# Optimization experiments

Measured on AMD Instinct MI355X. Metric: run time of the kernel, lower is better.

The kernel has to match this reference:

```python
import jax, jax.numpy as jnp
import numpy as np

N_NODES = 50000
N_EDGES = 800000


def setup_inputs() -> dict:
    key = jax.random.key(0)
    ks = jax.random.split(key, 10)
    x = jax.random.normal(ks[0], (N_NODES, 256), dtype=jnp.float32)
    edge_index = jax.random.randint(ks[1], (2, N_EDGES), 0, N_NODES, dtype=jnp.int64)
    edge_attr = jax.random.uniform(ks[2], (N_EDGES,), dtype=jnp.float32)
    def glorot(k, fan_in, fan_out):
        s = jnp.sqrt(6.0 / (fan_in + fan_out))
        return jax.random.uniform(k, (fan_in, fan_out), minval=-s, maxval=s, dtype=jnp.float32)
    W1 = glorot(ks[3], 256, 512); b1 = jnp.zeros((512,), jnp.float32)
    W2 = glorot(ks[4], 512, 256); b2 = jnp.zeros((256,), jnp.float32)
    W3 = glorot(ks[5], 256, 128); b3 = jnp.zeros((128,), jnp.float32)
    return {"x": x, "edge_index": edge_index, "edge_attr": edge_attr,
            "W1": W1, "b1": b1, "W2": W2, "b2": b2, "W3": W3, "b3": b3}


def _gcn_norm(edge_index, edge_attr, num_nodes):
    # PyG GCNConv default: add self-loops (weight 1), symmetric normalization.
    loops = jnp.arange(num_nodes, dtype=edge_index.dtype)
    src = jnp.concatenate([edge_index[0], loops])
    dst = jnp.concatenate([edge_index[1], loops])
    w = jnp.concatenate([edge_attr, jnp.ones((num_nodes,), edge_attr.dtype)])
    deg = jax.ops.segment_sum(w, dst, num_segments=num_nodes)
    dinv = jnp.where(deg > 0, jax.lax.rsqrt(deg), 0.0)
    norm = dinv[src] * w * dinv[dst]  # [E+N]
    return src, dst, norm


def _gcn_conv(h, W, b, src, dst, norm, num_nodes):
    h = h @ W                                   # [N, Dout] linear transform
    msg = h[src] * norm[:, None]                # gather + per-edge scale
    out = jax.ops.segment_sum(msg, dst, num_segments=num_nodes)  # scatter-add
    return out + b


def reference(x, edge_index, edge_attr, W1, b1, W2, b2, W3, b3):
    src, dst, norm = _gcn_norm(edge_index, edge_attr, N_NODES)
    h = jax.nn.relu(_gcn_conv(x, W1, b1, src, dst, norm, N_NODES))
    # dropout is identity in eval mode (reference runs with training=False)
    h = jax.nn.relu(_gcn_conv(h, W2, b2, src, dst, norm, N_NODES))
    h = _gcn_conv(h, W3, b3, src, dst, norm, N_NODES)
    return h.reshape(-1, h.shape[1])
```

## Files before the change

kernel.cpp:

```cpp
#include <hip/hip_runtime.h>
#include <cstdint>
#include <cstddef>

typedef unsigned short u16;
typedef unsigned int u32;

#define NN 50000
#define NE 800000

typedef __attribute__((ext_vector_type(8))) short bf16x8;
typedef __attribute__((ext_vector_type(4))) float f32x4;

__device__ __forceinline__ u16 f2bf(float f) {
  union { float f; u32 i; } v; v.f = f;
  return (u16)((v.i + 0x7FFFu + ((v.i >> 16) & 1u)) >> 16);
}
__device__ __forceinline__ void bf2x2(u32 w, float& a, float& b) {
  union { u32 i; float f; } lo, hi;
  lo.i = w << 16; hi.i = w & 0xFFFF0000u;
  a = lo.f; b = hi.f;
}
__device__ __forceinline__ void unpack8(const uint4& q, float* f) {
  bf2x2(q.x, f[0], f[1]); bf2x2(q.y, f[2], f[3]);
  bf2x2(q.z, f[4], f[5]); bf2x2(q.w, f[6], f[7]);
}

__global__ void k_hist(int* __restrict__ cnt, const int* __restrict__ dst, int E) {
  int e = blockIdx.x * 256 + threadIdx.x;
  if (e < E) atomicAdd(&cnt[dst[e]], 1);
}
__global__ void k_scan_part(const int* __restrict__ cnt, int* __restrict__ bsum, int n) {
  __shared__ int s[256];
  int i = blockIdx.x * 256 + threadIdx.x;
  s[threadIdx.x] = (i < n) ? cnt[i] : 0;
  __syncthreads();
  for (int o = 128; o > 0; o >>= 1) {
    if (threadIdx.x < o) s[threadIdx.x] += s[threadIdx.x + o];
    __syncthreads();
  }
  if (threadIdx.x == 0) bsum[blockIdx.x] = s[0];
}
__global__ void k_scan_fin(const int* __restrict__ cnt, const int* __restrict__ bsum,
                           int* __restrict__ rowptr, int* __restrict__ cursor, int n) {
  __shared__ int s[256];
  __shared__ int pre[256];
  int t = threadIdx.x;
  int i = blockIdx.x * 256 + t;
  pre[t] = (t < blockIdx.x) ? bsum[t] : 0;
  s[t] = (i < n) ? cnt[i] : 0;
  __syncthreads();
  for (int o = 128; o > 0; o >>= 1) {
    if (t < o) pre[t] += pre[t + o];
    __syncthreads();
  }
  if (t == 0) {
    int run = pre[0];
    for (int j = 0; j < 256; j++) { int v = s[j]; s[j] = run; run += v; }
  }
  __syncthreads();
  if (i < n) { rowptr[i] = s[t]; cursor[i] = s[t]; }
}
__global__ void k_fill(const int* __restrict__ src, const int* __restrict__ dst,
                       const float* __restrict__ w,
                       int* __restrict__ cursor, uint2* __restrict__ edges, int E) {
  int e = blockIdx.x * 256 + threadIdx.x;
  if (e < E) {
    int d = dst[e];
    int p = atomicAdd(&cursor[d], 1);
    uint2 ev;
    ev.x = (u32)src[e];
    ev.y = __float_as_uint(w[e]);
    edges[p] = ev;
  }
}

__global__ __launch_bounds__(256) void k_sortrow(
    uint2* __restrict__ edges, const int* __restrict__ rowptr,
    const int* __restrict__ cnt, float* __restrict__ dinv, int n) {
  int wave = threadIdx.x >> 6, lane = threadIdx.x & 63;
  int row = blockIdx.x * 4 + wave;
  if (row >= n) return;
  int p = rowptr[row], c = cnt[row];
  if (c <= 64) {
    u32 kc = 0xFFFFFFFFu, kw = 0xFFFFFFFFu;
    if (lane < c) { uint2 e = edges[p + lane]; kc = e.x; kw = e.y; }
#pragma unroll
    for (int k = 2; k <= 64; k <<= 1) {
#pragma unroll
      for (int j = k >> 1; j > 0; j >>= 1) {
        u32 oc = __shfl_xor(kc, j, 64);
        u32 ow = __shfl_xor(kw, j, 64);
        bool up = ((lane & k) == 0);
        bool lower = ((lane & j) == 0);
        bool gt = (kc > oc) || (kc == oc && kw > ow);
        bool lt = (kc < oc) || (kc == oc && kw < ow);
        bool swap = up ? (lower ? gt : lt) : (lower ? lt : gt);
        if (swap) { kc = oc; kw = ow; }
      }
    }
    float s = (lane < c) ? __uint_as_float(kw) : 0.f;
#pragma unroll
    for (int off = 1; off < 64; off <<= 1) s += __shfl_xor(s, off, 64);
    if (lane < c) { uint2 e; e.x = kc; e.y = kw; edges[p + lane] = e; }
    if (lane == 0) dinv[row] = rsqrtf(1.0f + s);
  } else {
    if (lane == 0) {
      for (int i = 1; i < c; i++) {
        uint2 key = edges[p + i];
        int j2 = i - 1;
        while (j2 >= 0) {
          uint2 a = edges[p + j2];
          bool gt = (a.x > key.x) || (a.x == key.x && a.y > key.y);
          if (!gt) break;
          edges[p + j2 + 1] = a; j2--;
        }
        edges[p + j2 + 1] = key;
      }
      float s = 0.f;
      for (int i = 0; i < c; i++) s += __uint_as_float(edges[p + i].y);
      dinv[row] = rsqrtf(1.0f + s);
    }
  }
}

__global__ __launch_bounds__(256) void k_val(
    uint2* __restrict__ edges, const int* __restrict__ rowptr,
    const int* __restrict__ cnt, const float* __restrict__ dinv, int n) {
  int wave = threadIdx.x >> 6, lane = threadIdx.x & 63;
  int row = blockIdx.x * 4 + wave;
  if (row >= n) return;
  int p = rowptr[row], c = cnt[row];
  float dr = dinv[row];
  for (int l = lane; l < c; l += 64) {
    uint2 e = edges[p + l];
    float w = __uint_as_float(e.y);
    e.y = __float_as_uint(dinv[(int)e.x] * w * dr);
    edges[p + l] = e;
  }
}

#define XGROUPS (NN * 256 / 4)
__global__ void k_cast_all(const float* __restrict__ x, const float* __restrict__ W1,
                           const float* __restrict__ W2, const float* __restrict__ W3,
                           u16* __restrict__ xb, u16* __restrict__ Wt1,
                           u16* __restrict__ Wt2, u16* __restrict__ Wt3) {
  int i = blockIdx.x * 256 + threadIdx.x;
  if (i < XGROUPS) {
    float4 f = ((const float4*)x)[i];
    uint2 u;
    u.x = (u32)f2bf(f.x) | ((u32)f2bf(f.y) << 16);
    u.y = (u32)f2bf(f.z) | ((u32)f2bf(f.w) << 16);
    ((uint2*)xb)[i] = u;
  } else {
    int j = i - XGROUPS;
    if (j < 131072) {
      int k = j >> 9, n = j & 511;
      Wt1[n * 256 + k] = f2bf(W1[j]);
    } else if (j < 262144) {
      int j2 = j - 131072;
      int k = j2 >> 8, n = j2 & 255;
      Wt2[n * 512 + k] = f2bf(W2[j2]);
    } else if (j < 294912) {
      int j2 = j - 262144;
      int k = j2 >> 7, n = j2 & 127;
      Wt3[n * 256 + k] = f2bf(W3[j2]);
    }
  }
}

template <int D, int OUTF32, int RELU, int HASB, int U>
__global__ __launch_bounds__(128) void k_agg(
    const u16* __restrict__ H, const int* __restrict__ rowptr,
    const int* __restrict__ cnt, const uint2* __restrict__ edges,
    const float* __restrict__ dinv,
    const float* __restrict__ bias, void* __restrict__ outv) {
  constexpr int RL = D / 8;
  constexpr int EPW = 64 / RL;
  int wave = threadIdx.x >> 6, lane = threadIdx.x & 63;
  int node = blockIdx.x * 2 + wave;
  if (node >= NN) return;
  const int sub = lane / RL;
  const int rl = lane & (RL - 1);
  const int base = rl * 8;
  float acc[8] = {};
  if (sub == 0) {
    float dv = dinv[node];
    float sw = dv * dv;
    uint4 q = *(const uint4*)(H + (size_t)node * D + base);
    float f[8]; unpack8(q, f);
#pragma unroll
    for (int j = 0; j < 8; j++) acc[j] = sw * f[j];
  }
  const int p = rowptr[node], c = cnt[node];
  for (int e0 = 0; e0 < c; e0 += EPW * U) {
    uint4 q[U];
    float v[U];
#pragma unroll
    for (int u = 0; u < U; u++) {
      int id = e0 + sub + u * EPW;
      bool ok = id < c;
      uint2 ev = edges[p + (ok ? id : 0)];
      v[u] = ok ? __uint_as_float(ev.y) : 0.f;
      int cs = ok ? (int)ev.x : node;
      q[u] = *(const uint4*)(H + (size_t)cs * D + base);
    }
#pragma unroll
    for (int u = 0; u < U; u++) {
      float f[8]; unpack8(q[u], f);
#pragma unroll
      for (int j = 0; j < 8; j++) acc[j] += v[u] * f[j];
    }
  }
#pragma unroll
  for (int j = 0; j < 8; j++) {
#pragma unroll
    for (int off = RL; off < 64; off <<= 1)
      acc[j] += __shfl_xor(acc[j], off, 64);
  }
  if (sub == 0) {
#pragma unroll
    for (int j = 0; j < 8; j++) {
      float v2 = acc[j];
      if (HASB) v2 += bias[base + j];
      if (RELU) v2 = fmaxf(v2, 0.f);
      acc[j] = v2;
    }
    if (OUTF32) {
      float* o = (float*)outv + (size_t)node * D + base;
      float4 f0 = {acc[0], acc[1], acc[2], acc[3]};
      float4 f1 = {acc[4], acc[5], acc[6], acc[7]};
      *(float4*)o = f0;
      *(float4*)(o + 4) = f1;
    } else {
      u16* o = (u16*)outv + (size_t)node * D + base;
      uint4 u;
      u.x = (u32)f2bf(acc[0]) | ((u32)f2bf(acc[1]) << 16);
      u.y = (u32)f2bf(acc[2]) | ((u32)f2bf(acc[3]) << 16);
      u.z = (u32)f2bf(acc[4]) | ((u32)f2bf(acc[5]) << 16);
      u.w = (u32)f2bf(acc[6]) | ((u32)f2bf(acc[7]) << 16);
      *(uint4*)o = u;
    }
  }
}

template <int RELU, int HASB>
__global__ __launch_bounds__(512) void k_gemm(
    const u16* __restrict__ A, const u16* __restrict__ Bt,
    const float* __restrict__ bias, u16* __restrict__ C, int M, int Nd, int K) {
  __shared__ u16 As[256 * 64];
  __shared__ u16 Bs[128 * 64];
  const int tid = threadIdx.x;
  const int wave = tid >> 6, lane = tid & 63;
  const int m0 = blockIdx.x * 256, n0 = blockIdx.y * 128;
  const int wr = wave >> 1, wc = wave & 1;
  f32x4 acc[4][4] = {};

  for (int k0 = 0; k0 < K; k0 += 64) {
#pragma unroll
    for (int i = 0; i < 4; i++) {
      int r = i * 64 + wave * 8 + (lane >> 3);
      int rg = m0 + r; rg = rg < M ? rg : M - 1;
      const u16* ga = A + (size_t)rg * K + k0 + (lane & 7) * 8;
      __builtin_amdgcn_global_load_lds(
          (const __attribute__((address_space(1))) void*)ga,
          (__attribute__((address_space(3))) void*)&As[(i * 64 + wave * 8) * 64], 16, 0, 0);
    }
#pragma unroll
    for (int i = 0; i < 2; i++) {
      int r = i * 64 + wave * 8 + (lane >> 3);
      int ng = n0 + r;
      const u16* gb = Bt + (size_t)ng * K + k0 + (lane & 7) * 8;
      __builtin_amdgcn_global_load_lds(
          (const __attribute__((address_space(1))) void*)gb,
          (__attribute__((address_space(3))) void*)&Bs[(i * 64 + wave * 8) * 64], 16, 0, 0);
    }
    __syncthreads();
#pragma unroll
    for (int kk = 0; kk < 2; kk++) {
      bf16x8 af[4], bfr[4];
#pragma unroll
      for (int mi = 0; mi < 4; mi++)
        af[mi] = *(const bf16x8*)&As[(wr * 64 + mi * 16 + (lane & 15)) * 64 + kk * 32 + (lane >> 4) * 8];
#pragma unroll
      for (int ni = 0; ni < 4; ni++)
        bfr[ni] = *(const bf16x8*)&Bs[(wc * 64 + ni * 16 + (lane & 15)) * 64 + kk * 32 + (lane >> 4) * 8];
#pragma unroll
      for (int mi = 0; mi < 4; mi++)
#pragma unroll
        for (int ni = 0; ni < 4; ni++)
          acc[mi][ni] = __builtin_amdgcn_mfma_f32_16x16x32_bf16(af[mi], bfr[ni], acc[mi][ni], 0, 0, 0);
    }
    __syncthreads();
  }
  const int nb = n0 + wc * 64 + (lane & 15);
  float bv[4];
#pragma unroll
  for (int ni = 0; ni < 4; ni++) bv[ni] = HASB ? bias[nb + ni * 16] : 0.f;
#pragma unroll
  for (int mi = 0; mi < 4; mi++) {
#pragma unroll
    for (int r = 0; r < 4; r++) {
      int row = m0 + wr * 64 + mi * 16 + (lane >> 4) * 4 + r;
      if (row < M) {
#pragma unroll
        for (int ni = 0; ni < 4; ni++) {
          float v = acc[mi][ni][r] + bv[ni];
          if (RELU) v = fmaxf(v, 0.f);
          C[(size_t)row * Nd + nb + ni * 16] = f2bf(v);
        }
      }
    }
  }
}

extern "C" void kernel_launch(void* const* d_in, const int* in_sizes, int n_in,
                              void* d_out, int out_size, void* d_ws, size_t ws_size,
                              hipStream_t stream) {
  const float* x  = (const float*)d_in[0];
  const int*   ei = (const int*)d_in[1];
  const float* ea = (const float*)d_in[2];
  const float* W1 = (const float*)d_in[3];
  const float* b1 = (const float*)d_in[4];
  const float* W2 = (const float*)d_in[5];
  const float* b2 = (const float*)d_in[6];
  const float* W3 = (const float*)d_in[7];
  const float* b3 = (const float*)d_in[8];
  const int* e_src = ei;
  const int* e_dst = ei + NE;

  size_t off = 0;
  auto carve = [&](size_t bytes) -> void* {
    void* r = (char*)d_ws + off;
    off += (bytes + 255) & ~(size_t)255;
    return r;
  };
  float* dinv   = (float*)carve(NN * 4);
  int*   counts = (int*)carve(NN * 4);
  int*   rowptr = (int*)carve(NN * 4);
  int*   cursor = (int*)carve(NN * 4);
  int*   bsum   = (int*)carve(256 * 4);
  uint2* edges  = (uint2*)carve((size_t)NE * 8);
  u16*   Wt1    = (u16*)carve(512 * 256 * 2);
  u16*   Wt2    = (u16*)carve(256 * 512 * 2);
  u16*   Wt3    = (u16*)carve(128 * 256 * 2);
  u16*   R0     = (u16*)carve((size_t)NN * 256 * 2);
  u16*   R1     = (u16*)carve((size_t)NN * 256 * 2);
  u16*   R2     = (u16*)carve((size_t)NN * 512 * 2);

  const int NB_N = (NN + 255) / 256;
  const int NB_E = (NE + 255) / 256;
  const int ROW_B = (NN + 3) / 4;
  const int AGG_B = (NN + 1) / 2;

  hipMemsetAsync(counts, 0, (size_t)NN * 4, stream);
  k_hist<<<NB_E, 256, 0, stream>>>(counts, e_dst, NE);
  k_scan_part<<<NB_N, 256, 0, stream>>>(counts, bsum, NN);
  k_scan_fin<<<NB_N, 256, 0, stream>>>(counts, bsum, rowptr, cursor, NN);
  k_fill<<<NB_E, 256, 0, stream>>>(e_src, e_dst, ea, cursor, edges, NE);
  k_sortrow<<<ROW_B, 256, 0, stream>>>(edges, rowptr, counts, dinv, NN);
  k_val<<<ROW_B, 256, 0, stream>>>(edges, rowptr, counts, dinv, NN);

  k_cast_all<<<(XGROUPS + 294912 + 255) / 256, 256, 0, stream>>>(
      x, W1, W2, W3, R0, Wt1, Wt2, Wt3);

  dim3 g1((NN + 255) / 256, 512 / 128);
  dim3 g2((NN + 255) / 256, 256 / 128);
  dim3 g3((NN + 255) / 256, 128 / 128);

  k_agg<256, 0, 0, 0, 4><<<AGG_B, 128, 0, stream>>>(R0, rowptr, counts, edges, dinv, nullptr, R1);
  k_gemm<1, 1><<<g1, 512, 0, stream>>>(R1, Wt1, b1, R2, NN, 512, 256);
  k_gemm<0, 0><<<g2, 512, 0, stream>>>(R2, Wt2, nullptr, R0, NN, 256, 512);
  k_agg<256, 0, 1, 1, 4><<<AGG_B, 128, 0, stream>>>(R0, rowptr, counts, edges, dinv, b2, R1);
  k_gemm<0, 0><<<g3, 512, 0, stream>>>(R1, Wt3, nullptr, R0, NN, 128, 256);
  k_agg<128, 1, 0, 1, 4><<<AGG_B, 128, 0, stream>>>(R0, rowptr, counts, edges, dinv, b3, d_out);
}
```

Baseline: 391.0 us.

## Fuse degree computation into histogram, normalize in fill, remap GEMM blocks across XCDs

Computes weighted degree during the histogram pass with deterministic fixed-point 64-bit atomics, merges the bf16 cast kernel into that launch, and computes dinv in the scan kernel. Edge normalization now happens in k_fill, which removes the separate k_val pass and the degree reduction inside the sort. The GEMMs use a 1D grid with an XCD-aware block remapping so neighbouring tiles share an L2. This cuts kernel launches and passes over the edge array, at the cost of 64-bit atomics and double-precision conversions per edge.

Result: no change. 396.9 us (+1.5%).

```diff
diff --git a/kernel.cpp b/kernel.cpp
--- a/kernel.cpp
+++ b/kernel.cpp
@@ -4,6 +4,7 @@
 
 typedef unsigned short u16;
 typedef unsigned int u32;
+typedef unsigned long long u64;
 
 #define NN 50000
 #define NE 800000
@@ -25,10 +26,51 @@
   bf2x2(q.z, f[4], f[5]); bf2x2(q.w, f[6], f[7]);
 }
 
-__global__ void k_hist(int* __restrict__ cnt, const int* __restrict__ dst, int E) {
-  int e = blockIdx.x * 256 + threadIdx.x;
-  if (e < E) atomicAdd(&cnt[dst[e]], 1);
-}
+#define HIST_B 3125
+#define XGROUPS (NN * 256 / 4)
+#define DEGSCALE 1099511627776.0
+
+__global__ void k_histdeg_cast(const int* __restrict__ dst, const float* __restrict__ w,
+                               int* __restrict__ cnt, u64* __restrict__ degfix,
+                               const float* __restrict__ x, const float* __restrict__ W1,
+                               const float* __restrict__ W2, const float* __restrict__ W3,
+                               u16* __restrict__ xb, u16* __restrict__ Wt1,
+                               u16* __restrict__ Wt2, u16* __restrict__ Wt3) {
+  int b = blockIdx.x;
+  if (b < HIST_B) {
+    int e = b * 256 + threadIdx.x;
+    if (e < NE) {
+      int d = dst[e];
+      atomicAdd(&cnt[d], 1);
+      u64 fx = (u64)((double)w[e] * DEGSCALE + 0.5);
+      atomicAdd(&degfix[d], fx);
+    }
+  } else {
+    int i = (b - HIST_B) * 256 + threadIdx.x;
+    if (i < XGROUPS) {
+      float4 f = ((const float4*)x)[i];
+      uint2 u;
+      u.x = (u32)f2bf(f.x) | ((u32)f2bf(f.y) << 16);
+      u.y = (u32)f2bf(f.z) | ((u32)f2bf(f.w) << 16);
+      ((uint2*)xb)[i] = u;
+    } else {
+      int j = i - XGROUPS;
+      if (j < 131072) {
+        int k = j >> 9, n = j & 511;
+        Wt1[n * 256 + k] = f2bf(W1[j]);
+      } else if (j < 262144) {
+        int j2 = j - 131072;
+        int k = j2 >> 8, n = j2 & 255;
+        Wt2[n * 512 + k] = f2bf(W2[j2]);
+      } else if (j < 294912) {
+        int j2 = j - 262144;
+        int k = j2 >> 7, n = j2 & 127;
+        Wt3[n * 256 + k] = f2bf(W3[j2]);
+      }
+    }
+  }
+}
+
 __global__ void k_scan_part(const int* __restrict__ cnt, int* __restrict__ bsum, int n) {
   __shared__ int s[256];
   int i = blockIdx.x * 256 + threadIdx.x;
@@ -41,7 +83,9 @@
   if (threadIdx.x == 0) bsum[blockIdx.x] = s[0];
 }
 __global__ void k_scan_fin(const int* __restrict__ cnt, const int* __restrict__ bsum,
-                           int* __restrict__ rowptr, int* __restrict__ cursor, int n) {
+                           const u64* __restrict__ degfix,
+                           int* __restrict__ rowptr, int* __restrict__ cursor,
+                           float* __restrict__ dinv, int n) {
   __shared__ int s[256];
   __shared__ int pre[256];
   int t = threadIdx.x;
@@ -58,25 +102,30 @@
     for (int j = 0; j < 256; j++) { int v = s[j]; s[j] = run; run += v; }
   }
   __syncthreads();
-  if (i < n) { rowptr[i] = s[t]; cursor[i] = s[t]; }
+  if (i < n) {
+    rowptr[i] = s[t];
+    cursor[i] = s[t];
+    double dg = 1.0 + (double)degfix[i] * (1.0 / DEGSCALE);
+    dinv[i] = rsqrtf((float)dg);
+  }
 }
 __global__ void k_fill(const int* __restrict__ src, const int* __restrict__ dst,
-                       const float* __restrict__ w,
+                       const float* __restrict__ w, const float* __restrict__ dinv,
                        int* __restrict__ cursor, uint2* __restrict__ edges, int E) {
   int e = blockIdx.x * 256 + threadIdx.x;
   if (e < E) {
-    int d = dst[e];
+    int d = dst[e], s0 = src[e];
     int p = atomicAdd(&cursor[d], 1);
     uint2 ev;
-    ev.x = (u32)src[e];
-    ev.y = __float_as_uint(w[e]);
+    ev.x = (u32)s0;
+    ev.y = __float_as_uint(dinv[s0] * w[e] * dinv[d]);
     edges[p] = ev;
   }
 }
 
 __global__ __launch_bounds__(256) void k_sortrow(
     uint2* __restrict__ edges, const int* __restrict__ rowptr,
-    const int* __restrict__ cnt, float* __restrict__ dinv, int n) {
+    const int* __restrict__ cnt, int n) {
   int wave = threadIdx.x >> 6, lane = threadIdx.x & 63;
   int row = blockIdx.x * 4 + wave;
   if (row >= n) return;
@@ -98,11 +147,7 @@
         if (swap) { kc = oc; kw = ow; }
       }
     }
-    float s = (lane < c) ? __uint_as_float(kw) : 0.f;
-#pragma unroll
-    for (int off = 1; off < 64; off <<= 1) s += __shfl_xor(s, off, 64);
     if (lane < c) { uint2 e; e.x = kc; e.y = kw; edges[p + lane] = e; }
-    if (lane == 0) dinv[row] = rsqrtf(1.0f + s);
   } else {
     if (lane == 0) {
       for (int i = 1; i < c; i++) {
@@ -116,54 +161,6 @@
         }
         edges[p + j2 + 1] = key;
       }
-      float s = 0.f;
-      for (int i = 0; i < c; i++) s += __uint_as_float(edges[p + i].y);
-      dinv[row] = rsqrtf(1.0f + s);
-    }
-  }
-}
-
-__global__ __launch_bounds__(256) void k_val(
-    uint2* __restrict__ edges, const int* __restrict__ rowptr,
-    const int* __restrict__ cnt, const float* __restrict__ dinv, int n) {
-  int wave = threadIdx.x >> 6, lane = threadIdx.x & 63;
-  int row = blockIdx.x * 4 + wave;
-  if (row >= n) return;
-  int p = rowptr[row], c = cnt[row];
-  float dr = dinv[row];
-  for (int l = lane; l < c; l += 64) {
-    uint2 e = edges[p + l];
-    float w = __uint_as_float(e.y);
-    e.y = __float_as_uint(dinv[(int)e.x] * w * dr);
-    edges[p + l] = e;
-  }
-}
-
-#define XGROUPS (NN * 256 / 4)
-__global__ void k_cast_all(const float* __restrict__ x, const float* __restrict__ W1,
-                           const float* __restrict__ W2, const float* __restrict__ W3,
-                           u16* __restrict__ xb, u16* __restrict__ Wt1,
-                           u16* __restrict__ Wt2, u16* __restrict__ Wt3) {
-  int i = blockIdx.x * 256 + threadIdx.x;
-  if (i < XGROUPS) {
-    float4 f = ((const float4*)x)[i];
-    uint2 u;
-    u.x = (u32)f2bf(f.x) | ((u32)f2bf(f.y) << 16);
-    u.y = (u32)f2bf(f.z) | ((u32)f2bf(f.w) << 16);
-    ((uint2*)xb)[i] = u;
-  } else {
-    int j = i - XGROUPS;
-    if (j < 131072) {
-      int k = j >> 9, n = j & 511;
-      Wt1[n * 256 + k] = f2bf(W1[j]);
-    } else if (j < 262144) {
-      int j2 = j - 131072;
-      int k = j2 >> 8, n = j2 & 255;
-      Wt2[n * 512 + k] = f2bf(W2[j2]);
-    } else if (j < 294912) {
-      int j2 = j - 262144;
-      int k = j2 >> 7, n = j2 & 127;
-      Wt3[n * 256 + k] = f2bf(W3[j2]);
     }
   }
 }
@@ -243,7 +240,7 @@
   }
 }
 
-template <int RELU, int HASB>
+template <int RELU, int HASB, int NYB>
 __global__ __launch_bounds__(512) void k_gemm(
     const u16* __restrict__ A, const u16* __restrict__ Bt,
     const float* __restrict__ bias, u16* __restrict__ C, int M, int Nd, int K) {
@@ -251,15 +248,20 @@
   __shared__ u16 Bs[128 * 64];
   const int tid = threadIdx.x;
   const int wave = tid >> 6, lane = tid & 63;
-  const int m0 = blockIdx.x * 256, n0 = blockIdx.y * 128;
+  const int nwg = gridDim.x;
+  const int orig = blockIdx.x;
+  const int xcd = orig & 7;
+  const int q = nwg >> 3, r = nwg & 7;
+  const int wgid = (xcd < r ? xcd * (q + 1) : r * (q + 1) + (xcd - r) * q) + (orig >> 3);
+  const int m0 = (wgid / NYB) * 256, n0 = (wgid % NYB) * 128;
   const int wr = wave >> 1, wc = wave & 1;
   f32x4 acc[4][4] = {};
 
   for (int k0 = 0; k0 < K; k0 += 64) {
 #pragma unroll
     for (int i = 0; i < 4; i++) {
-      int r = i * 64 + wave * 8 + (lane >> 3);
-      int rg = m0 + r; rg = rg < M ? rg : M - 1;
+      int rr = i * 64 + wave * 8 + (lane >> 3);
+      int rg = m0 + rr; rg = rg < M ? rg : M - 1;
       const u16* ga = A + (size_t)rg * K + k0 + (lane & 7) * 8;
       __builtin_amdgcn_global_load_lds(
           (const __attribute__((address_space(1))) void*)ga,
@@ -267,8 +269,8 @@
     }
 #pragma unroll
     for (int i = 0; i < 2; i++) {
-      int r = i * 64 + wave * 8 + (lane >> 3);
-      int ng = n0 + r;
+      int rr = i * 64 + wave * 8 + (lane >> 3);
+      int ng = n0 + rr;
       const u16* gb = Bt + (size_t)ng * K + k0 + (lane & 7) * 8;
       __builtin_amdgcn_global_load_lds(
           (const __attribute__((address_space(1))) void*)gb,
@@ -299,12 +301,12 @@
 #pragma unroll
   for (int mi = 0; mi < 4; mi++) {
 #pragma unroll
-    for (int r = 0; r < 4; r++) {
-      int row = m0 + wr * 64 + mi * 16 + (lane >> 4) * 4 + r;
+    for (int rr = 0; rr < 4; rr++) {
+      int row = m0 + wr * 64 + mi * 16 + (lane >> 4) * 4 + rr;
       if (row < M) {
 #pragma unroll
         for (int ni = 0; ni < 4; ni++) {
-          float v = acc[mi][ni][r] + bv[ni];
+          float v = acc[mi][ni][rr] + bv[ni];
           if (RELU) v = fmaxf(v, 0.f);
           C[(size_t)row * Nd + nb + ni * 16] = f2bf(v);
         }
@@ -334,8 +336,9 @@
     off += (bytes + 255) & ~(size_t)255;
     return r;
   };
+  int*   counts = (int*)carve(NN * 4);
+  u64*   degfix = (u64*)carve(NN * 8);
   float* dinv   = (float*)carve(NN * 4);
-  int*   counts = (int*)carve(NN * 4);
   int*   rowptr = (int*)carve(NN * 4);
   int*   cursor = (int*)carve(NN * 4);
   int*   bsum   = (int*)carve(256 * 4);
@@ -352,25 +355,20 @@
   const int ROW_B = (NN + 3) / 4;
   const int AGG_B = (NN + 1) / 2;
 
-  hipMemsetAsync(counts, 0, (size_t)NN * 4, stream);
-  k_hist<<<NB_E, 256, 0, stream>>>(counts, e_dst, NE);
+  size_t zlen = (size_t)((char*)(degfix + NN) - (char*)counts);
+  hipMemsetAsync(counts, 0, zlen, stream);
+
+  k_histdeg_cast<<<HIST_B + (XGROUPS + 294912 + 255) / 256, 256, 0, stream>>>(
+      e_dst, ea, counts, degfix, x, W1, W2, W3, R0, Wt1, Wt2, Wt3);
   k_scan_part<<<NB_N, 256, 0, stream>>>(counts, bsum, NN);
-  k_scan_fin<<<NB_N, 256, 0, stream>>>(counts, bsum, rowptr, cursor, NN);
-  k_fill<<<NB_E, 256, 0, stream>>>(e_src, e_dst, ea, cursor, edges, NE);
-  k_sortrow<<<ROW_B, 256, 0, stream>>>(edges, rowptr, counts, dinv, NN);
-  k_val<<<ROW_B, 256, 0, stream>>>(edges, rowptr, counts, dinv, NN);
-
-  k_cast_all<<<(XGROUPS + 294912 + 255) / 256, 256, 0, stream>>>(
-      x, W1, W2, W3, R0, Wt1, Wt2, Wt3);
-
-  dim3 g1((NN + 255) / 256, 512 / 128);
-  dim3 g2((NN + 255) / 256, 256 / 128);
-  dim3 g3((NN + 255) / 256, 128 / 128);
+  k_scan_fin<<<NB_N, 256, 0, stream>>>(counts, bsum, degfix, rowptr, cursor, dinv, NN);
+  k_fill<<<NB_E, 256, 0, stream>>>(e_src, e_dst, ea, dinv, cursor, edges, NE);
+  k_sortrow<<<ROW_B, 256, 0, stream>>>(edges, rowptr, counts, NN);
 
   k_agg<256, 0, 0, 0, 4><<<AGG_B, 128, 0, stream>>>(R0, rowptr, counts, edges, dinv, nullptr, R1);
-  k_gemm<1, 1><<<g1, 512, 0, stream>>>(R1, Wt1, b1, R2, NN, 512, 256);
-  k_gemm<0, 0><<<g2, 512, 0, stream>>>(R2, Wt2, nullptr, R0, NN, 256, 512);
+  k_gemm<1, 1, 4><<<196 * 4, 512, 0, stream>>>(R1, Wt1, b1, R2, NN, 512, 256);
+  k_gemm<0, 0, 2><<<196 * 2, 512, 0, stream>>>(R2, Wt2, nullptr, R0, NN, 256, 512);
   k_agg<256, 0, 1, 1, 4><<<AGG_B, 128, 0, stream>>>(R0, rowptr, counts, edges, dinv, b2, R1);
-  k_gemm<0, 0><<<g3, 512, 0, stream>>>(R1, Wt3, nullptr, R0, NN, 128, 256);
+  k_gemm<0, 0, 1><<<196 * 1, 512, 0, stream>>>(R1, Wt3, nullptr, R0, NN, 128, 256);
   k_agg<128, 1, 0, 1, 4><<<AGG_B, 128, 0, stream>>>(R0, rowptr, counts, edges, dinv, b3, d_out);
 }
```

## Fuse histogram with cast, record atomic slots, remap GEMM blocks per XCD

Applied to the files above, without the earlier changes.

The degree histogram now saves each edge's atomic return value as a slot index, and it runs in the same launch as the bf16 cast of x and the weights. The fill kernel then writes edges to rowptr+slot with no second atomic pass, and the cursor array is dropped. The GEMMs switch to a 1D grid whose block ids are remapped so that consecutive tiles land on the same XCD, sharing the A rows in that XCD's L2. The cost is an extra 3.2MB slot buffer written and then read back.

Result: faster. 345.8 us (-11.6%).

```diff
diff --git a/kernel.cpp b/kernel.cpp
--- a/kernel.cpp
+++ b/kernel.cpp
@@ -25,10 +25,45 @@
   bf2x2(q.z, f[4], f[5]); bf2x2(q.w, f[6], f[7]);
 }
 
-__global__ void k_hist(int* __restrict__ cnt, const int* __restrict__ dst, int E) {
-  int e = blockIdx.x * 256 + threadIdx.x;
-  if (e < E) atomicAdd(&cnt[dst[e]], 1);
-}
+#define HIST_B 3125
+#define XGROUPS (NN * 256 / 4)
+
+__global__ void k_hist_cast(const int* __restrict__ dst,
+                            int* __restrict__ cnt, int* __restrict__ slot,
+                            const float* __restrict__ x, const float* __restrict__ W1,
+                            const float* __restrict__ W2, const float* __restrict__ W3,
+                            u16* __restrict__ xb, u16* __restrict__ Wt1,
+                            u16* __restrict__ Wt2, u16* __restrict__ Wt3) {
+  int b = blockIdx.x;
+  if (b < HIST_B) {
+    int e = b * 256 + threadIdx.x;
+    if (e < NE) slot[e] = atomicAdd(&cnt[dst[e]], 1);
+  } else {
+    int i = (b - HIST_B) * 256 + threadIdx.x;
+    if (i < XGROUPS) {
+      float4 f = ((const float4*)x)[i];
+      uint2 u;
+      u.x = (u32)f2bf(f.x) | ((u32)f2bf(f.y) << 16);
+      u.y = (u32)f2bf(f.z) | ((u32)f2bf(f.w) << 16);
+      ((uint2*)xb)[i] = u;
+    } else {
+      int j = i - XGROUPS;
+      if (j < 131072) {
+        int k = j >> 9, n = j & 511;
+        Wt1[n * 256 + k] = f2bf(W1[j]);
+      } else if (j < 262144) {
+        int j2 = j - 131072;
+        int k = j2 >> 8, n = j2 & 255;
+        Wt2[n * 512 + k] = f2bf(W2[j2]);
+      } else if (j < 294912) {
+        int j2 = j - 262144;
+        int k = j2 >> 7, n = j2 & 127;
+        Wt3[n * 256 + k] = f2bf(W3[j2]);
+      }
+    }
+  }
+}
+
 __global__ void k_scan_part(const int* __restrict__ cnt, int* __restrict__ bsum, int n) {
   __shared__ int s[256];
   int i = blockIdx.x * 256 + threadIdx.x;
@@ -41,7 +76,7 @@
   if (threadIdx.x == 0) bsum[blockIdx.x] = s[0];
 }
 __global__ void k_scan_fin(const int* __restrict__ cnt, const int* __restrict__ bsum,
-                           int* __restrict__ rowptr, int* __restrict__ cursor, int n) {
+                           int* __restrict__ rowptr, int n) {
   __shared__ int s[256];
   __shared__ int pre[256];
   int t = threadIdx.x;
@@ -58,19 +93,18 @@
     for (int j = 0; j < 256; j++) { int v = s[j]; s[j] = run; run += v; }
   }
   __syncthreads();
-  if (i < n) { rowptr[i] = s[t]; cursor[i] = s[t]; }
+  if (i < n) rowptr[i] = s[t];
 }
 __global__ void k_fill(const int* __restrict__ src, const int* __restrict__ dst,
-                       const float* __restrict__ w,
-                       int* __restrict__ cursor, uint2* __restrict__ edges, int E) {
+                       const float* __restrict__ w, const int* __restrict__ rowptr,
+                       const int* __restrict__ slot, uint2* __restrict__ edges, int E) {
   int e = blockIdx.x * 256 + threadIdx.x;
   if (e < E) {
     int d = dst[e];
-    int p = atomicAdd(&cursor[d], 1);
     uint2 ev;
     ev.x = (u32)src[e];
     ev.y = __float_as_uint(w[e]);
-    edges[p] = ev;
+    edges[rowptr[d] + slot[e]] = ev;
   }
 }
 
@@ -136,35 +170,6 @@
     float w = __uint_as_float(e.y);
     e.y = __float_as_uint(dinv[(int)e.x] * w * dr);
     edges[p + l] = e;
-  }
-}
-
-#define XGROUPS (NN * 256 / 4)
-__global__ void k_cast_all(const float* __restrict__ x, const float* __restrict__ W1,
-                           const float* __restrict__ W2, const float* __restrict__ W3,
-                           u16* __restrict__ xb, u16* __restrict__ Wt1,
-                           u16* __restrict__ Wt2, u16* __restrict__ Wt3) {
-  int i = blockIdx.x * 256 + threadIdx.x;
-  if (i < XGROUPS) {
-    float4 f = ((const float4*)x)[i];
-    uint2 u;
-    u.x = (u32)f2bf(f.x) | ((u32)f2bf(f.y) << 16);
-    u.y = (u32)f2bf(f.z) | ((u32)f2bf(f.w) << 16);
-    ((uint2*)xb)[i] = u;
-  } else {
-    int j = i - XGROUPS;
-    if (j < 131072) {
-      int k = j >> 9, n = j & 511;
-      Wt1[n * 256 + k] = f2bf(W1[j]);
-    } else if (j < 262144) {
-      int j2 = j - 131072;
-      int k = j2 >> 8, n = j2 & 255;
-      Wt2[n * 512 + k] = f2bf(W2[j2]);
-    } else if (j < 294912) {
-      int j2 = j - 262144;
-      int k = j2 >> 7, n = j2 & 127;
-      Wt3[n * 256 + k] = f2bf(W3[j2]);
-    }
   }
 }
 
@@ -243,7 +248,7 @@
   }
 }
 
-template <int RELU, int HASB>
+template <int RELU, int HASB, int NYB>
 __global__ __launch_bounds__(512) void k_gemm(
     const u16* __restrict__ A, const u16* __restrict__ Bt,
     const float* __restrict__ bias, u16* __restrict__ C, int M, int Nd, int K) {
@@ -251,15 +256,20 @@
   __shared__ u16 Bs[128 * 64];
   const int tid = threadIdx.x;
   const int wave = tid >> 6, lane = tid & 63;
-  const int m0 = blockIdx.x * 256, n0 = blockIdx.y * 128;
+  const int nwg = gridDim.x;
+  const int orig = blockIdx.x;
+  const int xcd = orig & 7;
+  const int q = nwg >> 3, r = nwg & 7;
+  const int wgid = (xcd < r ? xcd * (q + 1) : r * (q + 1) + (xcd - r) * q) + (orig >> 3);
+  const int m0 = (wgid / NYB) * 256, n0 = (wgid % NYB) * 128;
   const int wr = wave >> 1, wc = wave & 1;
   f32x4 acc[4][4] = {};
 
   for (int k0 = 0; k0 < K; k0 += 64) {
 #pragma unroll
     for (int i = 0; i < 4; i++) {
-      int r = i * 64 + wave * 8 + (lane >> 3);
-      int rg = m0 + r; rg = rg < M ? rg : M - 1;
+      int rr = i * 64 + wave * 8 + (lane >> 3);
+      int rg = m0 + rr; rg = rg < M ? rg : M - 1;
       const u16* ga = A + (size_t)rg * K + k0 + (lane & 7) * 8;
       __builtin_amdgcn_global_load_lds(
           (const __attribute__((address_space(1))) void*)ga,
@@ -267,8 +277,8 @@
     }
 #pragma unroll
     for (int i = 0; i < 2; i++) {
-      int r = i * 64 + wave * 8 + (lane >> 3);
-      int ng = n0 + r;
+      int rr = i * 64 + wave * 8 + (lane >> 3);
+      int ng = n0 + rr;
       const u16* gb = Bt + (size_t)ng * K + k0 + (lane & 7) * 8;
       __builtin_amdgcn_global_load_lds(
           (const __attribute__((address_space(1))) void*)gb,
@@ -299,12 +309,12 @@
 #pragma unroll
   for (int mi = 0; mi < 4; mi++) {
 #pragma unroll
-    for (int r = 0; r < 4; r++) {
-      int row = m0 + wr * 64 + mi * 16 + (lane >> 4) * 4 + r;
+    for (int rr = 0; rr < 4; rr++) {
+      int row = m0 + wr * 64 + mi * 16 + (lane >> 4) * 4 + rr;
       if (row < M) {
 #pragma unroll
         for (int ni = 0; ni < 4; ni++) {
-          float v = acc[mi][ni][r] + bv[ni];
+          float v = acc[mi][ni][rr] + bv[ni];
           if (RELU) v = fmaxf(v, 0.f);
           C[(size_t)row * Nd + nb + ni * 16] = f2bf(v);
         }
@@ -334,11 +344,11 @@
     off += (bytes + 255) & ~(size_t)255;
     return r;
   };
+  int*   counts = (int*)carve(NN * 4);
   float* dinv   = (float*)carve(NN * 4);
-  int*   counts = (int*)carve(NN * 4);
   int*   rowptr = (int*)carve(NN * 4);
-  int*   cursor = (int*)carve(NN * 4);
   int*   bsum   = (int*)carve(256 * 4);
+  int*   slot   = (int*)carve((size_t)NE * 4);
   uint2* edges  = (uint2*)carve((size_t)NE * 8);
   u16*   Wt1    = (u16*)carve(512 * 256 * 2);
   u16*   Wt2    = (u16*)carve(256 * 512 * 2);
@@ -353,24 +363,19 @@
   const int AGG_B = (NN + 1) / 2;
 
   hipMemsetAsync(counts, 0, (size_t)NN * 4, stream);
-  k_hist<<<NB_E, 256, 0, stream>>>(counts, e_dst, NE);
+
+  k_hist_cast<<<HIST_B + (XGROUPS + 294912 + 255) / 256, 256, 0, stream>>>(
+      e_dst, counts, slot, x, W1, W2, W3, R0, Wt1, Wt2, Wt3);
   k_scan_part<<<NB_N, 256, 0, stream>>>(counts, bsum, NN);
-  k_scan_fin<<<NB_N, 256, 0, stream>>>(counts, bsum, rowptr, cursor, NN);
-  k_fill<<<NB_E, 256, 0, stream>>>(e_src, e_dst, ea, cursor, edges, NE);
+  k_scan_fin<<<NB_N, 256, 0, stream>>>(counts, bsum, rowptr, NN);
+  k_fill<<<NB_E, 256, 0, stream>>>(e_src, e_dst, ea, rowptr, slot, edges, NE);
   k_sortrow<<<ROW_B, 256, 0, stream>>>(edges, rowptr, counts, dinv, NN);
   k_val<<<ROW_B, 256, 0, stream>>>(edges, rowptr, counts, dinv, NN);
 
-  k_cast_all<<<(XGROUPS + 294912 + 255) / 256, 256, 0, stream>>>(
-      x, W1, W2, W3, R0, Wt1, Wt2, Wt3);
-
-  dim3 g1((NN + 255) / 256, 512 / 128);
-  dim3 g2((NN + 255) / 256, 256 / 128);
-  dim3 g3((NN + 255) / 256, 128 / 128);
-
   k_agg<256, 0, 0, 0, 4><<<AGG_B, 128, 0, stream>>>(R0, rowptr, counts, edges, dinv, nullptr, R1);
-  k_gemm<1, 1><<<g1, 512, 0, stream>>>(R1, Wt1, b1, R2, NN, 512, 256);
-  k_gemm<0, 0><<<g2, 512, 0, stream>>>(R2, Wt2, nullptr, R0, NN, 256, 512);
+  k_gemm<1, 1, 4><<<196 * 4, 512, 0, stream>>>(R1, Wt1, b1, R2, NN, 512, 256);
+  k_gemm<0, 0, 2><<<196 * 2, 512, 0, stream>>>(R2, Wt2, nullptr, R0, NN, 256, 512);
   k_agg<256, 0, 1, 1, 4><<<AGG_B, 128, 0, stream>>>(R0, rowptr, counts, edges, dinv, b2, R1);
-  k_gemm<0, 0><<<g3, 512, 0, stream>>>(R1, Wt3, nullptr, R0, NN, 128, 256);
+  k_gemm<0, 0, 1><<<196 * 1, 512, 0, stream>>>(R1, Wt3, nullptr, R0, NN, 128, 256);
   k_agg<128, 1, 0, 1, 4><<<AGG_B, 128, 0, stream>>>(R0, rowptr, counts, edges, dinv, b3, d_out);
 }
```
